# Optimization experiments

Measured on AMD Instinct MI355X. Metric: run time of the kernel, lower is better.

The kernel has to match this reference:

```python
import jax, jax.numpy as jnp
import numpy as np

N = 4096
K = 32
K_NEIGH = 5
LR_EDGE = 0.05
LR_GLOBAL_DECAY = 0.001
NOISE_STD = 0.05
RIPPLE_STRENGTH = 0.01
SPARK_ENERGY_DECAY = 0.98
SPARK_FORCE_STEPS = 5
SPARK_MIN_ENERGY = 0.05
STATE_DECAY = 0.95


def setup_inputs() -> dict:
    key = jax.random.key(0)
    k1, k2, k3 = jax.random.split(key, 3)
    return {
        "W": 0.1 * jax.random.normal(k1, (N, N), jnp.float32),
        "s": jnp.zeros((N,), jnp.float32),
        "noise": jax.random.normal(k2, (N,), jnp.float32),
        "spark_energy": jnp.ones((K,), jnp.float32),
        "u": jax.random.uniform(k3, (K,), jnp.float32),
        "spark_pos": jnp.arange(K, dtype=jnp.int32) % N,
        "spark_age": jnp.zeros((K,), jnp.int32),
    }


def _step(W, s, noise, spark_energy, u, spark_pos, spark_age):
    n = W.shape[0]
    k = spark_pos.shape[0]
    # state diffusion: decay, noisy matvec, sigmoid
    s = s * STATE_DECAY
    s = jax.nn.sigmoid(W @ s + NOISE_STD * noise)
    # force young sparks' positions to 1.0 (drop-mode scatter for masked writes)
    force_idx = jnp.where(spark_age < SPARK_FORCE_STEPS, spark_pos, n)
    s = s.at[force_idx].set(1.0, mode="drop")

    def body(carry, xs):
        W, s = carry
        i, prev, energy, age, ui = xs
        # multinomial over relu(W[prev]) via inverse-CDF on cumsum
        row = W[prev]
        w = jax.nn.relu(row) + 1e-6
        cdf = jnp.cumsum(w)
        nxt = jnp.minimum(
            jnp.searchsorted(cdf, ui * cdf[-1], side="right"), n - 1
        ).astype(prev.dtype)
        # edge learning on traversed edge
        W = W.at[nxt, prev].set(W[nxt, prev] * (1.0 - LR_EDGE) + s[prev] * LR_EDGE)
        # ripple to top-K neighbors of prev (row re-read AFTER edge update, as in torch)
        top = jax.lax.top_k(jax.nn.relu(W[prev]), K_NEIGH)[1]
        W = W.at[prev, top].add(RIPPLE_STRENGTH)
        W = W.at[top, prev].add(RIPPLE_STRENGTH * 0.5)
        W = W.at[top[:, None], top[None, :]].add(RIPPLE_STRENGTH * 0.3)
        # energy decay, deposit energy at new position
        energy = energy * SPARK_ENERGY_DECAY
        s = s.at[nxt].set(energy)
        age = age + 1
        # respawn exhausted sparks
        respawn = energy < SPARK_MIN_ENERGY
        pos_new = jnp.where(respawn, (i % n).astype(prev.dtype), nxt)
        energy = jnp.where(respawn, jnp.float32(1.0), energy)
        age = jnp.where(respawn, jnp.int32(0), age)
        return (W, s), (pos_new, energy, age)

    idx = jnp.arange(k, dtype=jnp.int32)
    (W, s), (pos, energy, age) = jax.lax.scan(
        body, (W, s), (idx, spark_pos, spark_energy, spark_age, u)
    )
    # global decay + clamp
    W = jnp.clip(W * (1.0 - LR_GLOBAL_DECAY), -2.0, 2.0)
    return s, W, pos, energy, age


def reference(W, s, noise, spark_energy, u, spark_pos, spark_age):
    return _step(W, s, noise, spark_energy, u, spark_pos, spark_age)
```

## Files before the change

### kernel.cpp

```cpp
#include <hip/hip_runtime.h>

#define NN 4096
#define KS 32
#define KN 5

typedef float f32x4 __attribute__((ext_vector_type(4)));

#define WS_NXT   16384
#define WS_TOPI  16512
#define WS_NEED  (size_t)(WS_TOPI + KS * KN * 4)

__device__ __forceinline__ void merge5(float* av, int* ai,
                                       const float* bv2, const int* bi2) {
    float nv[KN]; int ni[KN];
    int pA = 0, pB = 0;
    #pragma unroll
    for (int q = 0; q < KN; ++q) {
        float va = av[pA];  int ia = ai[pA];
        float vb = bv2[pB]; int ib = bi2[pB];
        bool pickA = (va > vb) || (va == vb && ia < ib);
        if (pickA) { nv[q] = va; ni[q] = ia; ++pA; }
        else       { nv[q] = vb; ni[q] = ib; ++pB; }
    }
    #pragma unroll
    for (int q = 0; q < KN; ++q) { av[q] = nv[q]; ai[q] = ni[q]; }
}

__device__ __forceinline__ void cdf_scan(const float r[4], int tid, int lane, int wid,
                                         double* wave_incl, double incl[4],
                                         double& a_out, double& ascan_out) {
    double a = 0.0;
    #pragma unroll
    for (int m = 0; m < 4; ++m) {
        a += (double)(fmaxf(r[m], 0.f) + 1e-6f);
        incl[m] = a;
    }
    double ascan = a;
    #pragma unroll
    for (int off = 1; off < 64; off <<= 1) {
        double o = __shfl_up(ascan, (unsigned)off, 64);
        if (lane >= off) ascan += o;
    }
    if (lane == 63) wave_incl[wid] = ascan;
    __syncthreads();
    if (tid < 16) {
        double v = wave_incl[tid];
        #pragma unroll
        for (int off = 1; off < 16; off <<= 1) {
            double o = __shfl_up(v, (unsigned)off, 64);
            if (tid >= off) v += o;
        }
        wave_incl[tid] = v;
    }
    __syncthreads();
    a_out = a;
    ascan_out = ascan;
}

__device__ __forceinline__ void block_top5(const float r[4], int tid, int lane, int wid,
                                           float* topv, int* topi, int* dest) {
    float bv[KN]; int bi[KN];
    #pragma unroll
    for (int m = 0; m < 4; ++m) { bv[m] = fmaxf(r[m], 0.f); bi[m] = tid * 4 + m; }
    bv[4] = -1.f; bi[4] = 0x7fffffff;
    #define CE(i, j) { if (bv[i] < bv[j] || (bv[i] == bv[j] && bi[i] > bi[j])) { \
        float tv = bv[i]; bv[i] = bv[j]; bv[j] = tv; \
        int   ti = bi[i]; bi[i] = bi[j]; bi[j] = ti; } }
    CE(0, 1) CE(2, 3) CE(0, 2) CE(1, 3) CE(1, 2)
    #undef CE
    #pragma unroll
    for (int off = 1; off < 64; off <<= 1) {
        float ov[KN]; int oi[KN];
        #pragma unroll
        for (int q = 0; q < KN; ++q) {
            ov[q] = __shfl_xor(bv[q], off, 64);
            oi[q] = __shfl_xor(bi[q], off, 64);
        }
        merge5(bv, bi, ov, oi);
    }
    if (lane == 0) {
        #pragma unroll
        for (int q = 0; q < KN; ++q) { topv[wid * KN + q] = bv[q]; topi[wid * KN + q] = bi[q]; }
    }
    __syncthreads();
    if (tid < 16) {
        #pragma unroll
        for (int q = 0; q < KN; ++q) { bv[q] = topv[tid * KN + q]; bi[q] = topi[tid * KN + q]; }
        #pragma unroll
        for (int off = 1; off < 16; off <<= 1) {
            float ov[KN]; int oi[KN];
            #pragma unroll
            for (int q = 0; q < KN; ++q) {
                ov[q] = __shfl_xor(bv[q], off, 64);
                oi[q] = __shfl_xor(bi[q], off, 64);
            }
            merge5(bv, bi, ov, oi);
        }
        if (tid == 0) {
            #pragma unroll
            for (int q = 0; q < KN; ++q) dest[q] = bi[q];
        }
    }
    __syncthreads();
}

__global__ __launch_bounds__(256) void k_fused(const float* __restrict__ W,
                                               const float* __restrict__ s,
                                               const float* __restrict__ noise,
                                               float* __restrict__ s_out,
                                               float* __restrict__ outW) {
    __shared__ float sdec[NN];
    int tid = threadIdx.x;

    size_t base = (size_t)blockIdx.x * 1024 + tid;
    const f32x4* Wv = (const f32x4*)W;
    f32x4* Ov = (f32x4*)outW;
    f32x4 v0 = Wv[base];
    f32x4 v1 = Wv[base + 256];
    f32x4 v2 = Wv[base + 512];
    f32x4 v3 = Wv[base + 768];
    #define DC(v) { \
        v.x = fminf(fmaxf(v.x * 0.999f, -2.f), 2.f); \
        v.y = fminf(fmaxf(v.y * 0.999f, -2.f), 2.f); \
        v.z = fminf(fmaxf(v.z * 0.999f, -2.f), 2.f); \
        v.w = fminf(fmaxf(v.w * 0.999f, -2.f), 2.f); }
    DC(v0) DC(v1) DC(v2) DC(v3)
    #undef DC
    __builtin_nontemporal_store(v0, &Ov[base]);
    __builtin_nontemporal_store(v1, &Ov[base + 256]);
    __builtin_nontemporal_store(v2, &Ov[base + 512]);
    __builtin_nontemporal_store(v3, &Ov[base + 768]);

    if (blockIdx.x < NN / 4) {
        int nz = 0;
        for (int it = 0; it < 4; ++it) {
            float4 sv = ((const float4*)s)[it * 256 + tid];
            if (sv.x != 0.f || sv.y != 0.f || sv.z != 0.f || sv.w != 0.f) nz = 1;
            float4 d;
            d.x = sv.x * 0.95f; d.y = sv.y * 0.95f;
            d.z = sv.z * 0.95f; d.w = sv.w * 0.95f;
            ((float4*)sdec)[it * 256 + tid] = d;
        }
        int anynz = __syncthreads_or(nz);
        int wave = tid >> 6, lane = tid & 63;
        int row = blockIdx.x * 4 + wave;
        float acc = 0.f;
        if (anynz) {
            const float4* Wr = (const float4*)(W + (size_t)row * NN);
            for (int it = 0; it < 16; ++it) {
                float4 w = Wr[it * 64 + lane];
                int j = (it * 64 + lane) * 4;
                acc += w.x * sdec[j] + w.y * sdec[j + 1] + w.z * sdec[j + 2] + w.w * sdec[j + 3];
            }
        }
        for (int off = 32; off > 0; off >>= 1) acc += __shfl_down(acc, off, 64);
        if (lane == 0) {
            float y = acc + 0.05f * noise[row];
            s_out[row] = 1.0f / (1.0f + expf(-y));
        }
    }
}

__global__ __launch_bounds__(1024) void k_pre(const float* __restrict__ W,
                                              const int* __restrict__ pos_in,
                                              const float* __restrict__ u_in,
                                              char* __restrict__ wsb) {
    __shared__ double wave_incl[16];
    __shared__ float  topv[16 * KN];
    __shared__ int    topi[16 * KN];
    __shared__ int    sh_nxt;
    int tid = threadIdx.x, lane = tid & 63, wid = tid >> 6;
    int prev = pos_in[blockIdx.x];

    float4 rv = *((const float4*)(W + (size_t)prev * NN) + tid);
    float r[4] = {rv.x, rv.y, rv.z, rv.w};

    if (tid == 0) sh_nxt = NN - 1;
    double incl[4], a, ascan;
    cdf_scan(r, tid, lane, wid, wave_incl, incl, a, ascan);
    double waveExcl = (wid == 0) ? 0.0 : wave_incl[wid - 1];
    double total    = wave_incl[15];
    double thrIncl  = waveExcl + ascan;
    double thrExcl  = thrIncl - a;
    double t = (double)u_in[blockIdx.x] * total;
    if (thrIncl > t && thrExcl <= t) {
        int found = 3;
        #pragma unroll
        for (int m = 0; m < 4; ++m)
            if (thrExcl + incl[m] > t) { found = m; break; }
        sh_nxt = tid * 4 + found;
    }
    __syncthreads();
    if (tid == 0) ((int*)(wsb + WS_NXT))[blockIdx.x] = sh_nxt;

    block_top5(r, tid, lane, wid, topv, topi,
               (int*)(wsb + WS_TOPI) + blockIdx.x * KN);
}

__global__ __launch_bounds__(1024) void k_scan(float* __restrict__ W,
                                               const float* __restrict__ s_in,
                                               const float* __restrict__ energy_in,
                                               const float* __restrict__ u_in,
                                               const int* __restrict__ pos_in,
                                               const int* __restrict__ age_in,
                                               float* __restrict__ out,
                                               const char* __restrict__ wsb,
                                               int use_pre) {
    __shared__ float  s_lds[NN];
    __shared__ double wave_incl[16];
    __shared__ float  topv[16 * KN];
    __shared__ int    topi[16 * KN];
    __shared__ int    sh_top[KN];
    __shared__ int    sh_nxt;
    __shared__ unsigned int modlist[KS * 36];
    __shared__ float  res_pos[KS], res_en[KS], res_age[KS];
    __shared__ int    sh_pos[KS], sh_age[KS];
    __shared__ float  sh_u[KS], sh_en[KS];
    __shared__ unsigned char dirty[NN];
    __shared__ int    prenxt_lds[KS];
    __shared__ int    topi_lds[KS * KN];

    int tid = threadIdx.x;
    int lane = tid & 63, wid = tid >> 6;

    ((float4*)s_lds)[tid] = ((const float4*)s_in)[tid];
    ((unsigned int*)dirty)[tid] = 0u;
    if (tid < KS) {
        sh_pos[tid] = pos_in[tid];
        sh_age[tid] = age_in[tid];
        sh_u[tid]   = u_in[tid];
        sh_en[tid]  = energy_in[tid];
    }
    if (use_pre) {
        if (tid < KS)      prenxt_lds[tid] = ((const int*)(wsb + WS_NXT))[tid];
        if (tid < KS * KN) topi_lds[tid]   = ((const int*)(wsb + WS_TOPI))[tid];
    }
    __syncthreads();
    if (tid < KS && sh_age[tid] < 5) s_lds[sh_pos[tid]] = 1.0f;
    __syncthreads();

    for (int k = 0; k < KS; ++k) {
        int prev = sh_pos[k];
        bool rowClean = (use_pre != 0) && (dirty[prev] == 0);
        float r[4] = {0.f, 0.f, 0.f, 0.f};
        bool haveRow = false;
        int nxt;

        if (!rowClean) {
            float4 rv = *((const float4*)(W + (size_t)prev * NN) + tid);
            r[0] = rv.x; r[1] = rv.y; r[2] = rv.z; r[3] = rv.w;
            haveRow = true;
            if (tid == 0) sh_nxt = NN - 1;
            double incl[4], a, ascan;
            cdf_scan(r, tid, lane, wid, wave_incl, incl, a, ascan);
            double waveExcl = (wid == 0) ? 0.0 : wave_incl[wid - 1];
            double total    = wave_incl[15];
            double thrIncl  = waveExcl + ascan;
            double thrExcl  = thrIncl - a;
            double t = (double)sh_u[k] * total;
            if (thrIncl > t && thrExcl <= t) {
                int found = 3;
                #pragma unroll
                for (int m = 0; m < 4; ++m)
                    if (thrExcl + incl[m] > t) { found = m; break; }
                sh_nxt = tid * 4 + found;
            }
            __syncthreads();
            nxt = sh_nxt;
        } else {
            nxt = prenxt_lds[k];
        }

        bool fullTop = !rowClean || (nxt == prev);
        if (fullTop && !haveRow) {
            float4 rv = *((const float4*)(W + (size_t)prev * NN) + tid);
            r[0] = rv.x; r[1] = rv.y; r[2] = rv.z; r[3] = rv.w;
            haveRow = true;
            __syncthreads();
        }

        float sprev = s_lds[prev];
        if (tid == 0) {
            size_t o = (size_t)nxt * NN + prev;
            W[o] = W[o] * 0.95f + sprev * 0.05f;
        }

        int t0, t1, t2, t3, t4;
        if (fullTop) {
            if (nxt == prev && tid == (prev >> 2)) {
                int m = prev & 3;
                r[m] = r[m] * 0.95f + sprev * 0.05f;
            }
            block_top5(r, tid, lane, wid, topv, topi, sh_top);
            t0 = sh_top[0]; t1 = sh_top[1]; t2 = sh_top[2]; t3 = sh_top[3]; t4 = sh_top[4];
        } else {
            t0 = topi_lds[k * KN + 0]; t1 = topi_lds[k * KN + 1];
            t2 = topi_lds[k * KN + 2]; t3 = topi_lds[k * KN + 3];
            t4 = topi_lds[k * KN + 4];
            bool edgeAlias = (nxt == t0) || (nxt == t1) || (nxt == t2) ||
                             (nxt == t3) || (nxt == t4);
            if (edgeAlias) __syncthreads();
        }
        #define TOPQ(q) (fullTop ? sh_top[q] : topi_lds[k * KN + (q)])

        bool alias = (prev == t0) || (prev == t1) || (prev == t2) || (prev == t3) || (prev == t4);

        if (alias) {
            if (tid < KN) W[(size_t)prev * NN + TOPQ(tid)] += 0.01f;
            __syncthreads();
            if (tid < KN) W[(size_t)TOPQ(tid) * NN + prev] += 0.005f;
            __syncthreads();
            if (tid < KN * KN) W[(size_t)TOPQ(tid / KN) * NN + TOPQ(tid % KN)] += 0.003f;
        } else {
            if (tid < KN) {
                W[(size_t)prev * NN + TOPQ(tid)] += 0.01f;
                W[(size_t)TOPQ(tid) * NN + prev] += 0.005f;
            }
            if (tid >= 64 && tid < 64 + KN * KN) {
                int q = tid - 64;
                W[(size_t)TOPQ(q / KN) * NN + TOPQ(q % KN)] += 0.003f;
            }
        }

        if (tid < 36) {
            int row, col;
            if (tid == 0)       { row = nxt;             col = prev; }
            else if (tid < 6)   { row = prev;            col = TOPQ(tid - 1); }
            else if (tid < 11)  { row = TOPQ(tid - 6);   col = prev; }
            else { int q = tid - 11; row = TOPQ(q / KN); col = TOPQ(q % KN); }
            modlist[k * 36 + tid] = (unsigned)(row * NN + col);
        }

        if (tid == 0) { dirty[nxt] = 1; dirty[prev] = 1; }
        if (tid >= 128 && tid < 128 + KN) dirty[TOPQ(tid - 128)] = 1;
        #undef TOPQ

        if (tid == 0) {
            float en = sh_en[k] * 0.98f;
            s_lds[nxt] = en;
            int age = sh_age[k] + 1;
            int posn = nxt;
            if (en < 0.05f) { posn = k % NN; en = 1.0f; age = 0; }
            res_pos[k] = (float)posn;
            res_en[k]  = en;
            res_age[k] = (float)age;
        }
        __syncthreads();
    }

    ((float4*)out)[tid] = ((float4*)s_lds)[tid];
    if (tid < KS) {
        float* tail = out + NN + (size_t)NN * NN;
        tail[tid]          = res_pos[tid];
        tail[KS + tid]     = res_en[tid];
        tail[2 * KS + tid] = res_age[tid];
    }
    float* outW = out + NN;
    for (int i = tid; i < KS * 36; i += 1024) {
        unsigned idx = modlist[i];
        float v = W[idx] * 0.999f;
        v = fminf(fmaxf(v, -2.f), 2.f);
        outW[idx] = v;
    }
}

extern "C" void kernel_launch(void* const* d_in, const int* in_sizes, int n_in,
                              void* d_out, int out_size, void* d_ws, size_t ws_size,
                              hipStream_t stream) {
    float*       W      = (float*)d_in[0];
    const float* s      = (const float*)d_in[1];
    const float* noise  = (const float*)d_in[2];
    const float* energy = (const float*)d_in[3];
    const float* u      = (const float*)d_in[4];
    const int*   pos    = (const int*)d_in[5];
    const int*   age    = (const int*)d_in[6];
    float*       out    = (float*)d_out;
    float*       s_ws   = (float*)d_ws;

    int use_pre = (ws_size >= WS_NEED) ? 1 : 0;

    k_fused<<<(NN * (size_t)NN) / (16 * 256), 256, 0, stream>>>(W, s, noise, s_ws, out + NN);
    if (use_pre)
        k_pre<<<KS, 1024, 0, stream>>>(W, pos, u, (char*)d_ws);
    k_scan<<<1, 1024, 0, stream>>>(W, s_ws, energy, u, pos, age, out,
                                   (const char*)d_ws, use_pre);
}
```

Baseline: 184.4 us.

## Merge decay/matvec and spark-precompute kernels; prefetch edit values in scan

Folds the decay/clamp + matvec kernel and the per-spark CDF/top-5 precompute kernel into one launch with 1024-thread blocks, so the 32 precompute blocks run alongside the bulk copy instead of after it. In the serial scan kernel, all 36 edit addresses per step are computed up front and their W values prefetched into shared memory. Steps whose touched rows are clean and non-aliasing then write the updated values directly, skipping the dependent global read-modify-write. This adds shared memory and a fair amount of branching complexity. The larger blocks also change occupancy for the streaming copy.

```diff
diff --git a/kernel.cpp b/kernel.cpp
--- a/kernel.cpp
+++ b/kernel.cpp
@@ -104,97 +104,82 @@
     __syncthreads();
 }
 
-__global__ __launch_bounds__(256) void k_fused(const float* __restrict__ W,
-                                               const float* __restrict__ s,
-                                               const float* __restrict__ noise,
-                                               float* __restrict__ s_out,
-                                               float* __restrict__ outW) {
-    __shared__ float sdec[NN];
-    int tid = threadIdx.x;
-
-    size_t base = (size_t)blockIdx.x * 1024 + tid;
-    const f32x4* Wv = (const f32x4*)W;
-    f32x4* Ov = (f32x4*)outW;
-    f32x4 v0 = Wv[base];
-    f32x4 v1 = Wv[base + 256];
-    f32x4 v2 = Wv[base + 512];
-    f32x4 v3 = Wv[base + 768];
-    #define DC(v) { \
-        v.x = fminf(fmaxf(v.x * 0.999f, -2.f), 2.f); \
-        v.y = fminf(fmaxf(v.y * 0.999f, -2.f), 2.f); \
-        v.z = fminf(fmaxf(v.z * 0.999f, -2.f), 2.f); \
-        v.w = fminf(fmaxf(v.w * 0.999f, -2.f), 2.f); }
-    DC(v0) DC(v1) DC(v2) DC(v3)
-    #undef DC
-    __builtin_nontemporal_store(v0, &Ov[base]);
-    __builtin_nontemporal_store(v1, &Ov[base + 256]);
-    __builtin_nontemporal_store(v2, &Ov[base + 512]);
-    __builtin_nontemporal_store(v3, &Ov[base + 768]);
-
-    if (blockIdx.x < NN / 4) {
-        int nz = 0;
-        for (int it = 0; it < 4; ++it) {
-            float4 sv = ((const float4*)s)[it * 256 + tid];
-            if (sv.x != 0.f || sv.y != 0.f || sv.z != 0.f || sv.w != 0.f) nz = 1;
-            float4 d;
-            d.x = sv.x * 0.95f; d.y = sv.y * 0.95f;
-            d.z = sv.z * 0.95f; d.w = sv.w * 0.95f;
-            ((float4*)sdec)[it * 256 + tid] = d;
-        }
-        int anynz = __syncthreads_or(nz);
-        int wave = tid >> 6, lane = tid & 63;
-        int row = blockIdx.x * 4 + wave;
-        float acc = 0.f;
-        if (anynz) {
-            const float4* Wr = (const float4*)(W + (size_t)row * NN);
-            for (int it = 0; it < 16; ++it) {
-                float4 w = Wr[it * 64 + lane];
-                int j = (it * 64 + lane) * 4;
-                acc += w.x * sdec[j] + w.y * sdec[j + 1] + w.z * sdec[j + 2] + w.w * sdec[j + 3];
-            }
-        }
-        for (int off = 32; off > 0; off >>= 1) acc += __shfl_down(acc, off, 64);
-        if (lane == 0) {
-            float y = acc + 0.05f * noise[row];
-            s_out[row] = 1.0f / (1.0f + expf(-y));
-        }
-    }
-}
-
-__global__ __launch_bounds__(1024) void k_pre(const float* __restrict__ W,
-                                              const int* __restrict__ pos_in,
-                                              const float* __restrict__ u_in,
-                                              char* __restrict__ wsb) {
+__global__ __launch_bounds__(1024) void k_front(const float* __restrict__ W,
+                                                const float* __restrict__ s,
+                                                const float* __restrict__ noise,
+                                                float* __restrict__ s_out,
+                                                float* __restrict__ outW,
+                                                const int* __restrict__ pos_in,
+                                                const float* __restrict__ u_in,
+                                                char* __restrict__ wsb) {
+    __shared__ float  sdec[NN];
     __shared__ double wave_incl[16];
     __shared__ float  topv[16 * KN];
     __shared__ int    topi[16 * KN];
     __shared__ int    sh_nxt;
     int tid = threadIdx.x, lane = tid & 63, wid = tid >> 6;
-    int prev = pos_in[blockIdx.x];
-
-    float4 rv = *((const float4*)(W + (size_t)prev * NN) + tid);
-    float r[4] = {rv.x, rv.y, rv.z, rv.w};
-
-    if (tid == 0) sh_nxt = NN - 1;
-    double incl[4], a, ascan;
-    cdf_scan(r, tid, lane, wid, wave_incl, incl, a, ascan);
-    double waveExcl = (wid == 0) ? 0.0 : wave_incl[wid - 1];
-    double total    = wave_incl[15];
-    double thrIncl  = waveExcl + ascan;
-    double thrExcl  = thrIncl - a;
-    double t = (double)u_in[blockIdx.x] * total;
-    if (thrIncl > t && thrExcl <= t) {
-        int found = 3;
-        #pragma unroll
-        for (int m = 0; m < 4; ++m)
-            if (thrExcl + incl[m] > t) { found = m; break; }
-        sh_nxt = tid * 4 + found;
-    }
-    __syncthreads();
-    if (tid == 0) ((int*)(wsb + WS_NXT))[blockIdx.x] = sh_nxt;
-
-    block_top5(r, tid, lane, wid, topv, topi,
-               (int*)(wsb + WS_TOPI) + blockIdx.x * KN);
+    int bid = blockIdx.x;
+
+    if (bid < 4096) {
+        size_t g = (size_t)bid * 1024 + tid;
+        f32x4 v = ((const f32x4*)W)[g];
+        v.x = fminf(fmaxf(v.x * 0.999f, -2.f), 2.f);
+        v.y = fminf(fmaxf(v.y * 0.999f, -2.f), 2.f);
+        v.z = fminf(fmaxf(v.z * 0.999f, -2.f), 2.f);
+        v.w = fminf(fmaxf(v.w * 0.999f, -2.f), 2.f);
+        __builtin_nontemporal_store(v, &((f32x4*)outW)[g]);
+
+        if (bid < 256) {
+            float4 sv = ((const float4*)s)[tid];
+            int nz = (sv.x != 0.f || sv.y != 0.f || sv.z != 0.f || sv.w != 0.f) ? 1 : 0;
+            float4 d;
+            d.x = sv.x * 0.95f; d.y = sv.y * 0.95f;
+            d.z = sv.z * 0.95f; d.w = sv.w * 0.95f;
+            ((float4*)sdec)[tid] = d;
+            int anynz = __syncthreads_or(nz);
+            int row = bid * 16 + wid;
+            float acc = 0.f;
+            if (anynz) {
+                const float4* Wr = (const float4*)(W + (size_t)row * NN);
+                for (int it = 0; it < 16; ++it) {
+                    float4 w = Wr[it * 64 + lane];
+                    int j = (it * 64 + lane) * 4;
+                    acc += w.x * sdec[j] + w.y * sdec[j + 1] + w.z * sdec[j + 2] + w.w * sdec[j + 3];
+                }
+            }
+            for (int off = 32; off > 0; off >>= 1) acc += __shfl_down(acc, off, 64);
+            if (lane == 0) {
+                float y = acc + 0.05f * noise[row];
+                s_out[row] = 1.0f / (1.0f + expf(-y));
+            }
+        }
+    } else {
+        int kk = bid - 4096;
+        int prev = pos_in[kk];
+        float4 rv = *((const float4*)(W + (size_t)prev * NN) + tid);
+        float r[4] = {rv.x, rv.y, rv.z, rv.w};
+
+        if (tid == 0) sh_nxt = NN - 1;
+        double incl[4], a, ascan;
+        cdf_scan(r, tid, lane, wid, wave_incl, incl, a, ascan);
+        double waveExcl = (wid == 0) ? 0.0 : wave_incl[wid - 1];
+        double total    = wave_incl[15];
+        double thrIncl  = waveExcl + ascan;
+        double thrExcl  = thrIncl - a;
+        double t = (double)u_in[kk] * total;
+        if (thrIncl > t && thrExcl <= t) {
+            int found = 3;
+            #pragma unroll
+            for (int m = 0; m < 4; ++m)
+                if (thrExcl + incl[m] > t) { found = m; break; }
+            sh_nxt = tid * 4 + found;
+        }
+        __syncthreads();
+        if (tid == 0) ((int*)(wsb + WS_NXT))[kk] = sh_nxt;
+
+        block_top5(r, tid, lane, wid, topv, topi,
+                   (int*)(wsb + WS_TOPI) + kk * KN);
+    }
 }
 
 __global__ __launch_bounds__(1024) void k_scan(float* __restrict__ W,
@@ -213,6 +198,7 @@
     __shared__ int    sh_top[KN];
     __shared__ int    sh_nxt;
     __shared__ unsigned int modlist[KS * 36];
+    __shared__ float  preval[KS * 36];
     __shared__ float  res_pos[KS], res_en[KS], res_age[KS];
     __shared__ int    sh_pos[KS], sh_age[KS];
     __shared__ float  sh_u[KS], sh_en[KS];
@@ -236,6 +222,21 @@
         if (tid < KS * KN) topi_lds[tid]   = ((const int*)(wsb + WS_TOPI))[tid];
     }
     __syncthreads();
+
+    if (use_pre) {
+        for (int i = tid; i < KS * 36; i += 1024) {
+            int k = i / 36, j = i - k * 36;
+            int pv = sh_pos[k], nx = prenxt_lds[k];
+            int row, col;
+            if (j == 0)       { row = nx;                      col = pv; }
+            else if (j < 6)   { row = pv;                      col = topi_lds[k * KN + j - 1]; }
+            else if (j < 11)  { row = topi_lds[k * KN + j - 6]; col = pv; }
+            else { int q = j - 11; row = topi_lds[k * KN + q / KN]; col = topi_lds[k * KN + q % KN]; }
+            unsigned a = (unsigned)(row * NN + col);
+            modlist[i] = a;
+            preval[i]  = W[a];
+        }
+    }
     if (tid < KS && sh_age[tid] < 5) s_lds[sh_pos[tid]] = 1.0f;
     __syncthreads();
 
@@ -279,61 +280,86 @@
             __syncthreads();
         }
 
-        float sprev = s_lds[prev];
-        if (tid == 0) {
-            size_t o = (size_t)nxt * NN + prev;
-            W[o] = W[o] * 0.95f + sprev * 0.05f;
-        }
-
-        int t0, t1, t2, t3, t4;
-        if (fullTop) {
-            if (nxt == prev && tid == (prev >> 2)) {
-                int m = prev & 3;
-                r[m] = r[m] * 0.95f + sprev * 0.05f;
-            }
-            block_top5(r, tid, lane, wid, topv, topi, sh_top);
-            t0 = sh_top[0]; t1 = sh_top[1]; t2 = sh_top[2]; t3 = sh_top[3]; t4 = sh_top[4];
-        } else {
+        int t0 = 0, t1 = 0, t2 = 0, t3 = 0, t4 = 0;
+        bool usePreval = false, edgeAlias = false;
+        if (!fullTop) {
             t0 = topi_lds[k * KN + 0]; t1 = topi_lds[k * KN + 1];
             t2 = topi_lds[k * KN + 2]; t3 = topi_lds[k * KN + 3];
             t4 = topi_lds[k * KN + 4];
-            bool edgeAlias = (nxt == t0) || (nxt == t1) || (nxt == t2) ||
-                             (nxt == t3) || (nxt == t4);
-            if (edgeAlias) __syncthreads();
-        }
-        #define TOPQ(q) (fullTop ? sh_top[q] : topi_lds[k * KN + (q)])
-
-        bool alias = (prev == t0) || (prev == t1) || (prev == t2) || (prev == t3) || (prev == t4);
-
-        if (alias) {
-            if (tid < KN) W[(size_t)prev * NN + TOPQ(tid)] += 0.01f;
-            __syncthreads();
-            if (tid < KN) W[(size_t)TOPQ(tid) * NN + prev] += 0.005f;
-            __syncthreads();
-            if (tid < KN * KN) W[(size_t)TOPQ(tid / KN) * NN + TOPQ(tid % KN)] += 0.003f;
+            edgeAlias = (nxt == t0) || (nxt == t1) || (nxt == t2) ||
+                        (nxt == t3) || (nxt == t4);
+            bool aliasP = (prev == t0) || (prev == t1) || (prev == t2) ||
+                          (prev == t3) || (prev == t4);
+            bool dn = (dirty[nxt] | dirty[t0] | dirty[t1] |
+                       dirty[t2]  | dirty[t3] | dirty[t4]) != 0;
+            usePreval = !dn && !edgeAlias && !aliasP;
+        }
+
+        float sprev = s_lds[prev];
+        if (usePreval) {
+            if (tid < 36) {
+                unsigned a = modlist[k * 36 + tid];
+                float v = preval[k * 36 + tid];
+                float nv = (tid == 0) ? (v * 0.95f + sprev * 0.05f)
+                         : (tid < 6)  ? (v + 0.01f)
+                         : (tid < 11) ? (v + 0.005f)
+                                      : (v + 0.003f);
+                W[a] = nv;
+            }
         } else {
-            if (tid < KN) {
-                W[(size_t)prev * NN + TOPQ(tid)] += 0.01f;
-                W[(size_t)TOPQ(tid) * NN + prev] += 0.005f;
-            }
-            if (tid >= 64 && tid < 64 + KN * KN) {
-                int q = tid - 64;
-                W[(size_t)TOPQ(q / KN) * NN + TOPQ(q % KN)] += 0.003f;
-            }
-        }
-
-        if (tid < 36) {
-            int row, col;
-            if (tid == 0)       { row = nxt;             col = prev; }
-            else if (tid < 6)   { row = prev;            col = TOPQ(tid - 1); }
-            else if (tid < 11)  { row = TOPQ(tid - 6);   col = prev; }
-            else { int q = tid - 11; row = TOPQ(q / KN); col = TOPQ(q % KN); }
-            modlist[k * 36 + tid] = (unsigned)(row * NN + col);
+            if (tid == 0) {
+                size_t o = (size_t)nxt * NN + prev;
+                W[o] = W[o] * 0.95f + sprev * 0.05f;
+            }
+            if (fullTop) {
+                if (nxt == prev && tid == (prev >> 2)) {
+                    int m = prev & 3;
+                    r[m] = r[m] * 0.95f + sprev * 0.05f;
+                }
+                block_top5(r, tid, lane, wid, topv, topi, sh_top);
+                t0 = sh_top[0]; t1 = sh_top[1]; t2 = sh_top[2];
+                t3 = sh_top[3]; t4 = sh_top[4];
+            } else {
+                if (edgeAlias) __syncthreads();
+            }
+            #define TOPQ(q) (fullTop ? sh_top[q] : topi_lds[k * KN + (q)])
+            bool alias = (prev == t0) || (prev == t1) || (prev == t2) ||
+                         (prev == t3) || (prev == t4);
+
+            if (alias) {
+                if (tid < KN) W[(size_t)prev * NN + TOPQ(tid)] += 0.01f;
+                __syncthreads();
+                if (tid < KN) W[(size_t)TOPQ(tid) * NN + prev] += 0.005f;
+                __syncthreads();
+                if (tid < KN * KN) W[(size_t)TOPQ(tid / KN) * NN + TOPQ(tid % KN)] += 0.003f;
+            } else {
+                if (tid < KN) {
+                    W[(size_t)prev * NN + TOPQ(tid)] += 0.01f;
+                    W[(size_t)TOPQ(tid) * NN + prev] += 0.005f;
+                }
+                if (tid >= 64 && tid < 64 + KN * KN) {
+                    int q = tid - 64;
+                    W[(size_t)TOPQ(q / KN) * NN + TOPQ(q % KN)] += 0.003f;
+                }
+            }
+
+            if (tid < 36) {
+                int row, col;
+                if (tid == 0)       { row = nxt;             col = prev; }
+                else if (tid < 6)   { row = prev;            col = TOPQ(tid - 1); }
+                else if (tid < 11)  { row = TOPQ(tid - 6);   col = prev; }
+                else { int q = tid - 11; row = TOPQ(q / KN); col = TOPQ(q % KN); }
+                modlist[k * 36 + tid] = (unsigned)(row * NN + col);
+            }
+            #undef TOPQ
         }
 
         if (tid == 0) { dirty[nxt] = 1; dirty[prev] = 1; }
-        if (tid >= 128 && tid < 128 + KN) dirty[TOPQ(tid - 128)] = 1;
-        #undef TOPQ
+        if (tid >= 128 && tid < 128 + KN) {
+            int q = tid - 128;
+            int tr = fullTop ? sh_top[q] : topi_lds[k * KN + q];
+            dirty[tr] = 1;
+        }
 
         if (tid == 0) {
             float en = sh_en[k] * 0.98f;
@@ -379,9 +405,8 @@
 
     int use_pre = (ws_size >= WS_NEED) ? 1 : 0;
 
-    k_fused<<<(NN * (size_t)NN) / (16 * 256), 256, 0, stream>>>(W, s, noise, s_ws, out + NN);
-    if (use_pre)
-        k_pre<<<KS, 1024, 0, stream>>>(W, pos, u, (char*)d_ws);
+    k_front<<<4096 + (use_pre ? KS : 0), 1024, 0, stream>>>(
+        W, s, noise, s_ws, out + NN, pos, u, (char*)d_ws);
     k_scan<<<1, 1024, 0, stream>>>(W, s_ws, energy, u, pos, age, out,
                                    (const char*)d_ws, use_pre);
 }
```

Measured after the change: 155.4 us. -15.8%, faster.
